# Performance work log

Measured on AMD Instinct MI355X. Metric: run time of the kernel, lower is better.

Reference implementation:

```python
import jax, jax.numpy as jnp
import numpy as np

N, B, S, CIN, E, H = 8192, 4, 2816, 64, 128, 8
HD = E // H


def setup_inputs() -> dict:
    key = jax.random.key(0)
    ks = jax.random.split(key, 8)
    b_ids = jnp.sort(jax.random.randint(ks[0], (N,), 0, B))
    other = jax.random.randint(ks[1], (N, 3), 0, 100)
    voxel_coords = jnp.concatenate([b_ids[:, None], other], axis=1).astype(jnp.int32)
    s = 0.02
    return {
        'pillar_features': jax.random.normal(ks[2], (N, CIN), jnp.float32),
        'voxel_coords': voxel_coords,
        'batch_size': B,
        'max_pillars': S,
        'pre_w': jax.random.normal(ks[3], (CIN, E), jnp.float32) * s,
        'pre_b': jnp.zeros((E,), jnp.float32),
        'in_w': jax.random.normal(ks[4], (E, 3 * E), jnp.float32) * s,
        'in_b': jnp.zeros((3 * E,), jnp.float32),
        'out_w': jax.random.normal(ks[5], (E, E), jnp.float32) * s,
        'out_b': jnp.zeros((E,), jnp.float32),
        'ln1_g': jnp.ones((E,), jnp.float32),
        'ln1_b': jnp.zeros((E,), jnp.float32),
        'w1': jax.random.normal(ks[6], (E, 2 * E), jnp.float32) * s,
        'b1': jnp.zeros((2 * E,), jnp.float32),
        'w2': jax.random.normal(ks[7], (2 * E, E), jnp.float32) * s,
        'b2': jnp.zeros((E,), jnp.float32),
        'ln2_g': jnp.ones((E,), jnp.float32),
        'ln2_b': jnp.zeros((E,), jnp.float32),
    }


def _ln(x, g, b):
    m = jnp.mean(x, axis=-1, keepdims=True)
    v = jnp.var(x, axis=-1, keepdims=True)
    return (x - m) / jnp.sqrt(v + 1e-5) * g + b


def reference(pillar_features, voxel_coords, batch_size, max_pillars,
              pre_w, pre_b, in_w, in_b, out_w, out_b,
              ln1_g, ln1_b, w1, b1, w2, b2, ln2_g, ln2_b):
    n = pillar_features.shape[0]
    b_ids = voxel_coords[:, 0].astype(jnp.int32)
    counts = jax.ops.segment_sum(jnp.ones((n,), jnp.int32), b_ids, num_segments=batch_size)
    starts = jnp.concatenate([jnp.zeros((1,), jnp.int32), jnp.cumsum(counts)[:-1]])
    pos = jnp.arange(n, dtype=jnp.int32) - starts[b_ids]  # index within each batch (coords sorted by batch)

    # pack ragged pillars -> padded [B, S, C]
    padded = jnp.zeros((batch_size, max_pillars, pillar_features.shape[-1]),
                       pillar_features.dtype).at[b_ids, pos].set(pillar_features)
    valid = jnp.arange(max_pillars)[None, :] < counts[:, None]  # [B, S], True = real pillar

    x = padded @ pre_w + pre_b  # [B, S, E]

    # multi-head self-attention with key padding mask
    qkv = x @ in_w + in_b
    q, k, v = jnp.split(qkv, 3, axis=-1)
    def heads(t):
        return t.reshape(batch_size, max_pillars, H, HD).transpose(0, 2, 1, 3)
    q, k, v = heads(q), heads(k), heads(v)
    scores = jnp.einsum('bhqd,bhkd->bhqk', q, k) / jnp.sqrt(jnp.float32(HD))
    scores = scores + jnp.where(valid[:, None, None, :], 0.0, -1e9)
    attn = jax.nn.softmax(scores, axis=-1)
    ctx = jnp.einsum('bhqk,bhkd->bhqd', attn, v)
    ctx = ctx.transpose(0, 2, 1, 3).reshape(batch_size, max_pillars, E)
    attn_out = ctx @ out_w + out_b

    x = _ln(x + attn_out, ln1_g, ln1_b)
    ffn = jax.nn.gelu(x @ w1 + b1, approximate=False) @ w2 + b2
    x = _ln(x + ffn, ln2_g, ln2_b)

    # unpack back to ragged [N_total, E]
    return x[b_ids, pos]
```

## Files before the change

### kernel.cpp

```cpp
#include <hip/hip_runtime.h>
#include <hip/hip_bf16.h>
#include <math.h>

#define CIN 64
#define E   128
#define H3  384
#define FF  256
#define NH  8
#define HD  16
#define NBATCH 4

typedef __attribute__((ext_vector_type(8))) short short8;
typedef __attribute__((ext_vector_type(16))) float f32x16;
typedef __attribute__((ext_vector_type(4))) uint uint4v;

static __device__ __forceinline__ ushort f2bf(float f) {
    uint u = __float_as_uint(f);
    return (ushort)((u + 0x7fffu + ((u >> 16) & 1u)) >> 16);
}
static __device__ __forceinline__ uint f2bf2(float lo, float hi) {
    uint r;
    asm("v_cvt_pk_bf16_f32 %0, %1, %2" : "=v"(r) : "v"(lo), "v"(hi));
    return r;
}
static __device__ __forceinline__ void plswap(uint& a, uint& b) {
    auto r = __builtin_amdgcn_permlane32_swap(a, b, false, false);
    a = r[0]; b = r[1];
}
static __device__ __forceinline__ short8 mk8(uint a, uint b, uint c, uint d) {
    uint4v v; v[0] = a; v[1] = b; v[2] = c; v[3] = d;
    return __builtin_bit_cast(short8, v);
}

__global__ __launch_bounds__(256) void k_wprep(const float* w0, const float* w1, const float* w2,
                                               const float* w3, const float* w4,
                                               ushort* f0, ushort* f1, ushort* f2,
                                               ushort* f3, ushort* f4,
                                               const int* __restrict__ coords, int n,
                                               int* __restrict__ starts) {
    const int m = blockIdx.y;
    const int t = blockIdx.x * 256 + threadIdx.x;
    if (m == 5) {
        if (t >= n) return;
        int cur = coords[t * 4];
        int prev = (t == 0) ? -1 : coords[(t - 1) * 4];
        for (int bb = prev + 1; bb <= cur; ++bb) starts[bb] = t;
        if (t == n - 1)
            for (int bb = cur + 1; bb <= NBATCH; ++bb) starts[bb] = n;
        return;
    }
    const int Ks[5] = {CIN, E, E, E, FF};
    const int Ms[5] = {E, H3, E, FF, E};
    const float* src = m == 0 ? w0 : m == 1 ? w1 : m == 2 ? w2 : m == 3 ? w3 : w4;
    ushort* dst = m == 0 ? f0 : m == 1 ? f1 : m == 2 ? f2 : m == 3 ? f3 : f4;
    const int K = Ks[m], M = Ms[m];
    const int CT = M / 32;
    const int total = (K / 16) * CT * 64;
    if (t >= total) return;
    const int lane = t & 63;
    const int ct = (t >> 6) % CT;
    const int kt = (t >> 6) / CT;
    const int col = ct * 32 + (lane & 31);
    const int k0 = kt * 16 + 8 * (lane >> 5);
    const float* sp = src + (size_t)k0 * M + col;
    uint a = f2bf2(sp[0], sp[(size_t)M]);
    uint b = f2bf2(sp[2 * (size_t)M], sp[3 * (size_t)M]);
    uint c = f2bf2(sp[4 * (size_t)M], sp[5 * (size_t)M]);
    uint d = f2bf2(sp[6 * (size_t)M], sp[7 * (size_t)M]);
    *(short8*)(dst + (size_t)t * 8) = mk8(a, b, c, d);
}

__global__ __launch_bounds__(256) void k_preqkv(const float* __restrict__ feat, const ushort* __restrict__ wf0,
        const float* __restrict__ pre_b, const ushort* __restrict__ wf1, const float* __restrict__ in_b,
        float* __restrict__ x, ushort* __restrict__ qh, ushort* __restrict__ kh, ushort* __restrict__ vt2,
        int n, int npk) {
    __shared__ ushort sxb[32][136];
    __shared__ ushort lv[4][32][34];
    const int rt = blockIdx.x;
    const int NT = n >> 6;
    const int tid = threadIdx.x, w = tid >> 6, lane = tid & 63;
    const int l31 = lane & 31, hi = lane >> 5;
    const int row = rt * 32 + l31;
    const int gt = rt >> 1, halfT = rt & 1;
    const float SC = 0.25f * 1.4426950408889634f;
    {
        const uint ONE2 = 0x3F803F80u;
        for (int it = tid; it < 512; it += 256) {
            const int hh = it >> 6, rloc = (it >> 2) & 15, seg = it & 3;
            *(uint4*)(vt2 + ((size_t)(hh * NT + gt) * 32 + 16 + rloc) * 64 + halfT * 32 + seg * 8) =
                make_uint4(ONE2, ONE2, ONE2, ONE2);
        }
    }
    {
        f32x16 acc;
#pragma unroll
        for (int i = 0; i < 16; ++i) acc[i] = 0.f;
#pragma unroll
        for (int kt = 0; kt < 4; ++kt) {
            const float* ap = feat + (size_t)row * CIN + kt * 16 + 8 * hi;
            const float4 a0 = *(const float4*)ap;
            const float4 a1 = *(const float4*)(ap + 4);
            const short8 af = mk8(f2bf2(a0.x, a0.y), f2bf2(a0.z, a0.w),
                                  f2bf2(a1.x, a1.y), f2bf2(a1.z, a1.w));
            const short8 bf = *(const short8*)(wf0 + ((size_t)(kt * 4 + w) * 64 + lane) * 8);
            acc = __builtin_amdgcn_mfma_f32_32x32x16_bf16(af, bf, acc, 0, 0, 0);
        }
        const int col = w * 32 + l31;
        const float bj = pre_b[col];
#pragma unroll
        for (int r = 0; r < 16; ++r) {
            const int rowl = (r & 3) + 8 * (r >> 2) + 4 * hi;
            const float v = acc[r] + bj;
            x[(size_t)(rt * 32 + rowl) * E + col] = v;
            sxb[rowl][col] = f2bf(v);
        }
    }
    __syncthreads();
#pragma unroll
    for (int c = 0; c < 3; ++c) {
        const int ct = w + 4 * c;
        f32x16 acc;
#pragma unroll
        for (int i = 0; i < 16; ++i) acc[i] = 0.f;
#pragma unroll
        for (int kt = 0; kt < 8; ++kt) {
            const short8 af = *(const short8*)(&sxb[l31][kt * 16 + 8 * hi]);
            const short8 bf = *(const short8*)(wf1 + ((size_t)(kt * 12 + ct) * 64 + lane) * 8);
            acc = __builtin_amdgcn_mfma_f32_32x32x16_bf16(af, bf, acc, 0, 0, 0);
        }
        const int colg = ct * 32 + l31;
        const float bj = in_b[colg];
        if (c == 0) {
            const int hh = colg >> 4, d = colg & 15;
#pragma unroll
            for (int r = 0; r < 16; r += 2) {
                const int rowl = (r & 3) + 8 * (r >> 2) + 4 * hi;
                const int grow = rt * 32 + rowl;
                const uint u = f2bf2((acc[r] + bj) * SC, (acc[r + 1] + bj) * SC);
                qh[((size_t)hh * npk + grow) * 16 + d] = (ushort)u;
                qh[((size_t)hh * npk + grow + 1) * 16 + d] = (ushort)(u >> 16);
            }
        } else if (c == 1) {
            const int cg2 = colg - E;
            const int hh = cg2 >> 4, d = cg2 & 15;
#pragma unroll
            for (int r = 0; r < 16; r += 2) {
                const int rowl = (r & 3) + 8 * (r >> 2) + 4 * hi;
                const int grow = rt * 32 + rowl;
                const uint u = f2bf2(acc[r] + bj, acc[r + 1] + bj);
                kh[((size_t)hh * npk + grow) * 16 + d] = (ushort)u;
                kh[((size_t)hh * npk + grow + 1) * 16 + d] = (ushort)(u >> 16);
            }
        } else {
#pragma unroll
            for (int r = 0; r < 16; ++r) {
                const int rowl = (r & 3) + 8 * (r >> 2) + 4 * hi;
                lv[w][l31][rowl] = f2bf(acc[r] + bj);
            }
            const int d = lane >> 1, half = lane & 1;
            const int dg = (ct - 8) * 32 + d;
            const int hh = dg >> 4, dl = dg & 15;
            const short8 v0 = *(const short8*)(&lv[w][d][16 * half]);
            const short8 v1 = *(const short8*)(&lv[w][d][16 * half + 8]);
            ushort* dst = vt2 + ((size_t)(hh * NT + gt) * 32 + dl) * 64 + halfT * 32 + 16 * half;
            *(short8*)dst = v0;
            *(short8*)(dst + 8) = v1;
        }
    }
}

__global__ __launch_bounds__(256) void k_attn15(const ushort* __restrict__ qh, const ushort* __restrict__ kh,
        const ushort* __restrict__ vt2, const int* __restrict__ starts, ushort* __restrict__ ctxb,
        int n, int npk) {
    __shared__ float po[4][32][17];
    const int NT = n >> 6;
    const int bid = blockIdx.x;
    const int h = bid & 7;
    const int bx = bid >> 3;
    const int tid = threadIdx.x, lane = tid & 63, w = tid >> 6;
    int b = -1, bt = 0, s = 0, e = 0, cum = 0;
    for (int bb = 0; bb < NBATCH; ++bb) {
        int sb = starts[bb], eb = starts[bb + 1];
        int t = (eb - (sb & ~31) + 31) >> 5;
        if (b < 0 && bx < cum + t) { b = bb; bt = bx - cum; s = sb; e = eb; }
        cum += t;
    }
    if (b < 0) return;
    const int q0 = (s & ~31) + bt * 32;
    const int l31 = lane & 31, hi = lane >> 5;
    const short8 qf = *(const short8*)(qh + ((size_t)h * npk + q0 + l31) * 16 + 8 * hi);
    const int ks64 = s & ~63;
    const int ntk = (e - ks64 + 63) >> 6;
    const int tw = (ntk + 3) >> 2;
    const int t0 = w * tw, t1 = min(ntk, t0 + tw);

    f32x16 o, z;
#pragma unroll
    for (int i = 0; i < 16; ++i) { o[i] = 0.f; z[i] = 0.f; }

    const ushort* kbase = kh + ((size_t)h * npk + ks64 + l31) * 16 + 8 * hi;
    const ushort* vbase = vt2 + ((size_t)(h * NT + (ks64 >> 6)) * 32 + l31) * 64 + 8 * hi;

    short8 ck0, ck1, cv0, cv1, cv2, cv3;
    if (t0 < t1) {
        const ushort* kp = kbase + (size_t)t0 * 1024;
        ck0 = *(const short8*)kp;
        ck1 = *(const short8*)(kp + 512);
        const ushort* vp = vbase + (size_t)t0 * 2048;
        cv0 = *(const short8*)(vp);
        cv1 = *(const short8*)(vp + 16);
        cv2 = *(const short8*)(vp + 32);
        cv3 = *(const short8*)(vp + 48);
    }
    for (int tt = t0; tt < t1; ++tt) {
        const int ptn = min(tt + 1, t1 - 1);
        const ushort* kpn = kbase + (size_t)ptn * 1024;
        const short8 nk0 = *(const short8*)kpn;
        const short8 nk1 = *(const short8*)(kpn + 512);
        const ushort* vpn = vbase + (size_t)ptn * 2048;
        const short8 nv0 = *(const short8*)(vpn);
        const short8 nv1 = *(const short8*)(vpn + 16);
        const short8 nv2 = *(const short8*)(vpn + 32);
        const short8 nv3 = *(const short8*)(vpn + 48);
        f32x16 sf0 = __builtin_amdgcn_mfma_f32_32x32x16_bf16(ck0, qf, z, 0, 0, 0);
        f32x16 sf1 = __builtin_amdgcn_mfma_f32_32x32x16_bf16(ck1, qf, z, 0, 0, 0);
        if (tt == 0 || tt == ntk - 1) {
            const int ktg = ks64 + 64 * tt;
#pragma unroll
            for (int r = 0; r < 16; ++r) {
                const int key = ktg + (r & 3) + 8 * (r >> 2) + 4 * hi;
                if (key < s || key >= e) sf0[r] = -1e30f;
                if (key + 32 < s || key + 32 >= e) sf1[r] = -1e30f;
            }
        }
#pragma unroll
        for (int r = 0; r < 16; ++r) sf0[r] = __builtin_amdgcn_exp2f(sf0[r]);
        {
            uint pA0 = f2bf2(sf0[0], sf0[1]),  pA1 = f2bf2(sf0[2], sf0[3]);
            uint pA2 = f2bf2(sf0[4], sf0[5]),  pA3 = f2bf2(sf0[6], sf0[7]);
            uint pA4 = f2bf2(sf0[8], sf0[9]),  pA5 = f2bf2(sf0[10], sf0[11]);
            uint pA6 = f2bf2(sf0[12], sf0[13]), pA7 = f2bf2(sf0[14], sf0[15]);
            plswap(pA0, pA2); plswap(pA1, pA3);
            plswap(pA4, pA6); plswap(pA5, pA7);
            __builtin_amdgcn_s_setprio(1);
            o = __builtin_amdgcn_mfma_f32_32x32x16_bf16(cv0, mk8(pA0, pA1, pA2, pA3), o, 0, 0, 0);
            o = __builtin_amdgcn_mfma_f32_32x32x16_bf16(cv1, mk8(pA4, pA5, pA6, pA7), o, 0, 0, 0);
            __builtin_amdgcn_s_setprio(0);
        }
#pragma unroll
        for (int r = 0; r < 16; ++r) sf1[r] = __builtin_amdgcn_exp2f(sf1[r]);
        {
            uint pB0 = f2bf2(sf1[0], sf1[1]),  pB1 = f2bf2(sf1[2], sf1[3]);
            uint pB2 = f2bf2(sf1[4], sf1[5]),  pB3 = f2bf2(sf1[6], sf1[7]);
            uint pB4 = f2bf2(sf1[8], sf1[9]),  pB5 = f2bf2(sf1[10], sf1[11]);
            uint pB6 = f2bf2(sf1[12], sf1[13]), pB7 = f2bf2(sf1[14], sf1[15]);
            plswap(pB0, pB2); plswap(pB1, pB3);
            plswap(pB4, pB6); plswap(pB5, pB7);
            __builtin_amdgcn_s_setprio(1);
            o = __builtin_amdgcn_mfma_f32_32x32x16_bf16(cv2, mk8(pB0, pB1, pB2, pB3), o, 0, 0, 0);
            o = __builtin_amdgcn_mfma_f32_32x32x16_bf16(cv3, mk8(pB4, pB5, pB6, pB7), o, 0, 0, 0);
            __builtin_amdgcn_s_setprio(0);
        }
        ck0 = nk0; ck1 = nk1;
        cv0 = nv0; cv1 = nv1; cv2 = nv2; cv3 = nv3;
    }
#pragma unroll
    for (int r = 0; r < 8; ++r) {
        const int d = (r & 3) + 8 * (r >> 2) + 4 * hi;
        po[w][l31][d] = o[r];
    }
    if (hi == 0) po[w][l31][16] = o[8];
    __syncthreads();
    const int q = tid & 31, d0 = (tid >> 5) * 2;
    const int rowq = q0 + q;
    if (rowq >= s && rowq < e) {
        float L = 0.f, a0 = 0.f, a1 = 0.f;
#pragma unroll
        for (int ww = 0; ww < 4; ++ww) {
            L += po[ww][q][16];
            a0 += po[ww][q][d0];
            a1 += po[ww][q][d0 + 1];
        }
        const float inv = 1.f / L;
        *(uint*)(ctxb + (size_t)rowq * E + h * HD + d0) = f2bf2(a0 * inv, a1 * inv);
    }
}

__global__ __launch_bounds__(256) void k_post(const ushort* __restrict__ ctxb, const ushort* __restrict__ wf2,
        const float* __restrict__ ob, const float* __restrict__ x,
        const float* __restrict__ g1, const float* __restrict__ be1,
        const ushort* __restrict__ wf3, const float* __restrict__ b1,
        const ushort* __restrict__ wf4, const float* __restrict__ b2,
        const float* __restrict__ g2, const float* __restrict__ be2,
        float* __restrict__ out, int n) {
    __shared__ float ly[32][132];
    __shared__ ushort sxb[32][136];
    __shared__ ushort hbt[32][264];
    const int rt = blockIdx.x;
    const int tid = threadIdx.x, w = tid >> 6, lane = tid & 63;
    const int l31 = lane & 31, hi = lane >> 5;
    const int row = rt * 32 + l31;
    {
        f32x16 acc;
#pragma unroll
        for (int i = 0; i < 16; ++i) acc[i] = 0.f;
#pragma unroll
        for (int kt = 0; kt < 8; ++kt) {
            const short8 af = *(const short8*)(ctxb + (size_t)row * E + kt * 16 + 8 * hi);
            const short8 bf = *(const short8*)(wf2 + ((size_t)(kt * 4 + w) * 64 + lane) * 8);
            acc = __builtin_amdgcn_mfma_f32_32x32x16_bf16(af, bf, acc, 0, 0, 0);
        }
        const int col = w * 32 + l31;
        const float bj = ob[col];
#pragma unroll
        for (int r = 0; r < 16; ++r) {
            const int rowl = (r & 3) + 8 * (r >> 2) + 4 * hi;
            ly[rowl][col] = acc[r] + bj + x[(size_t)(rt * 32 + rowl) * E + col];
        }
    }
    __syncthreads();
    {
        const int r = tid >> 3, j = tid & 7;
        float* lrow = ly[r];
        float v[16];
#pragma unroll
        for (int q = 0; q < 4; ++q) {
            const float4 t = *(const float4*)(lrow + 16 * j + 4 * q);
            v[4 * q] = t.x; v[4 * q + 1] = t.y; v[4 * q + 2] = t.z; v[4 * q + 3] = t.w;
        }
        float s = 0.f, ss = 0.f;
#pragma unroll
        for (int i = 0; i < 16; ++i) { s += v[i]; ss += v[i] * v[i]; }
        for (int m = 1; m < 8; m <<= 1) { s += __shfl_xor(s, m); ss += __shfl_xor(ss, m); }
        const float mean = s * (1.f / 128.f);
        const float var = ss * (1.f / 128.f) - mean * mean;
        const float rstd = rsqrtf(var + 1e-5f);
        float zv[16];
#pragma unroll
        for (int q = 0; q < 4; ++q) {
            const float4 gg = *(const float4*)(g1 + 16 * j + 4 * q);
            const float4 bb = *(const float4*)(be1 + 16 * j + 4 * q);
            zv[4 * q]     = (v[4 * q] - mean) * rstd * gg.x + bb.x;
            zv[4 * q + 1] = (v[4 * q + 1] - mean) * rstd * gg.y + bb.y;
            zv[4 * q + 2] = (v[4 * q + 2] - mean) * rstd * gg.z + bb.z;
            zv[4 * q + 3] = (v[4 * q + 3] - mean) * rstd * gg.w + bb.w;
            *(float4*)(lrow + 16 * j + 4 * q) = make_float4(zv[4 * q], zv[4 * q + 1], zv[4 * q + 2], zv[4 * q + 3]);
        }
        *(uint4*)(&sxb[r][16 * j]) =
            make_uint4(f2bf2(zv[0], zv[1]), f2bf2(zv[2], zv[3]), f2bf2(zv[4], zv[5]), f2bf2(zv[6], zv[7]));
        *(uint4*)(&sxb[r][16 * j + 8]) =
            make_uint4(f2bf2(zv[8], zv[9]), f2bf2(zv[10], zv[11]), f2bf2(zv[12], zv[13]), f2bf2(zv[14], zv[15]));
    }
    __syncthreads();
#pragma unroll
    for (int c = 0; c < 2; ++c) {
        const int ct = w + 4 * c;
        f32x16 acc;
#pragma unroll
        for (int i = 0; i < 16; ++i) acc[i] = 0.f;
#pragma unroll
        for (int kt = 0; kt < 8; ++kt) {
            const short8 af = *(const short8*)(&sxb[l31][kt * 16 + 8 * hi]);
            const short8 bf = *(const short8*)(wf3 + ((size_t)(kt * 8 + ct) * 64 + lane) * 8);
            acc = __builtin_amdgcn_mfma_f32_32x32x16_bf16(af, bf, acc, 0, 0, 0);
        }
        const int col = ct * 32 + l31;
        const float bj = b1[col];
#pragma unroll
        for (int r = 0; r < 16; ++r) {
            const int rowl = (r & 3) + 8 * (r >> 2) + 4 * hi;
            const float vv = acc[r] + bj;
            hbt[rowl][col] = f2bf(0.5f * vv * (1.f + erff(vv * 0.7071067811865475f)));
        }
    }
    __syncthreads();
    float res[16];
    {
        f32x16 acc;
#pragma unroll
        for (int i = 0; i < 16; ++i) acc[i] = 0.f;
#pragma unroll
        for (int kt = 0; kt < 16; ++kt) {
            const short8 af = *(const short8*)(&hbt[l31][kt * 16 + 8 * hi]);
            const short8 bf = *(const short8*)(wf4 + ((size_t)(kt * 4 + w) * 64 + lane) * 8);
            acc = __builtin_amdgcn_mfma_f32_32x32x16_bf16(af, bf, acc, 0, 0, 0);
        }
        const int col = w * 32 + l31;
        const float bj = b2[col];
#pragma unroll
        for (int r = 0; r < 16; ++r) {
            const int rowl = (r & 3) + 8 * (r >> 2) + 4 * hi;
            res[r] = acc[r] + bj + ly[rowl][col];
        }
    }
    __syncthreads();
    {
        const int col = w * 32 + l31;
#pragma unroll
        for (int r = 0; r < 16; ++r) {
            const int rowl = (r & 3) + 8 * (r >> 2) + 4 * hi;
            ly[rowl][col] = res[r];
        }
    }
    __syncthreads();
    {
        const int r = tid >> 3, j = tid & 7;
        const float* lrow = ly[r];
        float v[16];
#pragma unroll
        for (int q = 0; q < 4; ++q) {
            const float4 t = *(const float4*)(lrow + 16 * j + 4 * q);
            v[4 * q] = t.x; v[4 * q + 1] = t.y; v[4 * q + 2] = t.z; v[4 * q + 3] = t.w;
        }
        float s = 0.f, ss = 0.f;
#pragma unroll
        for (int i = 0; i < 16; ++i) { s += v[i]; ss += v[i] * v[i]; }
        for (int m = 1; m < 8; m <<= 1) { s += __shfl_xor(s, m); ss += __shfl_xor(ss, m); }
        const float mean = s * (1.f / 128.f);
        const float var = ss * (1.f / 128.f) - mean * mean;
        const float rstd = rsqrtf(var + 1e-5f);
        const int grow = rt * 32 + r;
#pragma unroll
        for (int q = 0; q < 4; ++q) {
            const float4 gg = *(const float4*)(g2 + 16 * j + 4 * q);
            const float4 bb = *(const float4*)(be2 + 16 * j + 4 * q);
            float4 o;
            o.x = (v[4 * q] - mean) * rstd * gg.x + bb.x;
            o.y = (v[4 * q + 1] - mean) * rstd * gg.y + bb.y;
            o.z = (v[4 * q + 2] - mean) * rstd * gg.z + bb.z;
            o.w = (v[4 * q + 3] - mean) * rstd * gg.w + bb.w;
            *(float4*)(out + (size_t)grow * E + 16 * j + 4 * q) = o;
        }
    }
}

extern "C" void kernel_launch(void* const* d_in, const int* in_sizes, int n_in,
                              void* d_out, int out_size, void* d_ws, size_t ws_size,
                              hipStream_t stream) {
    const float* feat   = (const float*)d_in[0];
    const int*   coords = (const int*)d_in[1];
    const float* pre_w  = (const float*)d_in[4];
    const float* pre_b  = (const float*)d_in[5];
    const float* in_w   = (const float*)d_in[6];
    const float* in_b   = (const float*)d_in[7];
    const float* out_w  = (const float*)d_in[8];
    const float* out_b  = (const float*)d_in[9];
    const float* ln1_g  = (const float*)d_in[10];
    const float* ln1_b  = (const float*)d_in[11];
    const float* w1     = (const float*)d_in[12];
    const float* b1     = (const float*)d_in[13];
    const float* w2     = (const float*)d_in[14];
    const float* b2     = (const float*)d_in[15];
    const float* ln2_g  = (const float*)d_in[16];
    const float* ln2_b  = (const float*)d_in[17];
    float* out = (float*)d_out;

    const int n = in_sizes[0] / CIN;
    const int RT = n / 32;
    const int npk = n + 64;
    const int NT = n / 64;

    char* wsb = (char*)d_ws;
    int* starts = (int*)wsb;
    float* x    = (float*)(wsb + 256);
    ushort* qh  = (ushort*)(x + (size_t)n * E);
    ushort* kh  = qh + (size_t)NH * npk * 16;
    ushort* vt2 = kh + (size_t)NH * npk * 16;
    ushort* ctxb = vt2 + (size_t)NH * NT * 32 * 64;
    ushort* wf0 = ctxb + (size_t)n * E;
    ushort* wf1 = wf0 + 4 * 4 * 64 * 8;
    ushort* wf2 = wf1 + 8 * 12 * 64 * 8;
    ushort* wf3 = wf2 + 8 * 4 * 64 * 8;
    ushort* wf4 = wf3 + 8 * 8 * 64 * 8;

    k_wprep<<<dim3(32, 6), dim3(256), 0, stream>>>(pre_w, in_w, out_w, w1, w2,
                                                   wf0, wf1, wf2, wf3, wf4, coords, n, starts);
    k_preqkv<<<dim3(RT), dim3(256), 0, stream>>>(feat, wf0, pre_b, wf1, in_b, x, qh, kh, vt2, n, npk);
    k_attn15<<<dim3((n / 32 + NBATCH) * NH), dim3(256), 0, stream>>>(qh, kh, vt2, starts, ctxb, n, npk);
    k_post<<<dim3(RT), dim3(256), 0, stream>>>(ctxb, wf2, out_b, x, ln1_g, ln1_b,
                                               wf3, b1, wf4, b2, ln2_g, ln2_b, out, n);
}
```

Measured before the change: 78.48 us.

## Restructure V tile layout into per-slice blocks and drop register prefetch

Changes the transposed V buffer layout so each 16-key slice of a 64-key tile sits in its own contiguous 32x16 block. Each wavefront's V fragment loads then read contiguous 512-byte spans instead of strided 128-byte rows. The attention loop also drops its software double-buffered register prefetch of K/V in favour of direct loads each iteration. That lowers register pressure but exposes load latency unless the compiler or occupancy hides it.

```diff
diff --git a/kernel.cpp b/kernel.cpp
--- a/kernel.cpp
+++ b/kernel.cpp
@@ -86,8 +86,10 @@
     {
         const uint ONE2 = 0x3F803F80u;
         for (int it = tid; it < 512; it += 256) {
-            const int hh = it >> 6, rloc = (it >> 2) & 15, seg = it & 3;
-            *(uint4*)(vt2 + ((size_t)(hh * NT + gt) * 32 + 16 + rloc) * 64 + halfT * 32 + seg * 8) =
+            const int hh = it >> 6, rem = it & 63;
+            const int sl = 2 * halfT + (rem >> 5);
+            const int rloc = (rem >> 1) & 15, seg = rem & 1;
+            *(uint4*)(vt2 + (((size_t)(hh * NT + gt) * 4 + sl) * 32 + 16 + rloc) * 16 + seg * 8) =
                 make_uint4(ONE2, ONE2, ONE2, ONE2);
         }
     }
@@ -160,16 +162,17 @@
             const int d = lane >> 1, half = lane & 1;
             const int dg = (ct - 8) * 32 + d;
             const int hh = dg >> 4, dl = dg & 15;
+            const int sl = 2 * halfT + half;
             const short8 v0 = *(const short8*)(&lv[w][d][16 * half]);
             const short8 v1 = *(const short8*)(&lv[w][d][16 * half + 8]);
-            ushort* dst = vt2 + ((size_t)(hh * NT + gt) * 32 + dl) * 64 + halfT * 32 + 16 * half;
+            ushort* dst = vt2 + (((size_t)(hh * NT + gt) * 4 + sl) * 32 + dl) * 16;
             *(short8*)dst = v0;
             *(short8*)(dst + 8) = v1;
         }
     }
 }
 
-__global__ __launch_bounds__(256) void k_attn15(const ushort* __restrict__ qh, const ushort* __restrict__ kh,
+__global__ __launch_bounds__(256) void k_attn17(const ushort* __restrict__ qh, const ushort* __restrict__ kh,
         const ushort* __restrict__ vt2, const int* __restrict__ starts, ushort* __restrict__ ctxb,
         int n, int npk) {
     __shared__ float po[4][32][17];
@@ -199,29 +202,17 @@
     for (int i = 0; i < 16; ++i) { o[i] = 0.f; z[i] = 0.f; }
 
     const ushort* kbase = kh + ((size_t)h * npk + ks64 + l31) * 16 + 8 * hi;
-    const ushort* vbase = vt2 + ((size_t)(h * NT + (ks64 >> 6)) * 32 + l31) * 64 + 8 * hi;
-
-    short8 ck0, ck1, cv0, cv1, cv2, cv3;
-    if (t0 < t1) {
-        const ushort* kp = kbase + (size_t)t0 * 1024;
-        ck0 = *(const short8*)kp;
-        ck1 = *(const short8*)(kp + 512);
-        const ushort* vp = vbase + (size_t)t0 * 2048;
-        cv0 = *(const short8*)(vp);
-        cv1 = *(const short8*)(vp + 16);
-        cv2 = *(const short8*)(vp + 32);
-        cv3 = *(const short8*)(vp + 48);
-    }
+    const ushort* vbase = vt2 + (size_t)(h * NT + (ks64 >> 6)) * 2048 + l31 * 16 + 8 * hi;
+
     for (int tt = t0; tt < t1; ++tt) {
-        const int ptn = min(tt + 1, t1 - 1);
-        const ushort* kpn = kbase + (size_t)ptn * 1024;
-        const short8 nk0 = *(const short8*)kpn;
-        const short8 nk1 = *(const short8*)(kpn + 512);
-        const ushort* vpn = vbase + (size_t)ptn * 2048;
-        const short8 nv0 = *(const short8*)(vpn);
-        const short8 nv1 = *(const short8*)(vpn + 16);
-        const short8 nv2 = *(const short8*)(vpn + 32);
-        const short8 nv3 = *(const short8*)(vpn + 48);
+        const ushort* kp = kbase + (size_t)tt * 1024;
+        const short8 ck0 = *(const short8*)kp;
+        const short8 ck1 = *(const short8*)(kp + 512);
+        const ushort* vt = vbase + (size_t)tt * 2048;
+        const short8 vf0 = *(const short8*)(vt);
+        const short8 vf1 = *(const short8*)(vt + 512);
+        const short8 vf2 = *(const short8*)(vt + 1024);
+        const short8 vf3 = *(const short8*)(vt + 1536);
         f32x16 sf0 = __builtin_amdgcn_mfma_f32_32x32x16_bf16(ck0, qf, z, 0, 0, 0);
         f32x16 sf1 = __builtin_amdgcn_mfma_f32_32x32x16_bf16(ck1, qf, z, 0, 0, 0);
         if (tt == 0 || tt == ntk - 1) {
@@ -243,8 +234,8 @@
             plswap(pA0, pA2); plswap(pA1, pA3);
             plswap(pA4, pA6); plswap(pA5, pA7);
             __builtin_amdgcn_s_setprio(1);
-            o = __builtin_amdgcn_mfma_f32_32x32x16_bf16(cv0, mk8(pA0, pA1, pA2, pA3), o, 0, 0, 0);
-            o = __builtin_amdgcn_mfma_f32_32x32x16_bf16(cv1, mk8(pA4, pA5, pA6, pA7), o, 0, 0, 0);
+            o = __builtin_amdgcn_mfma_f32_32x32x16_bf16(vf0, mk8(pA0, pA1, pA2, pA3), o, 0, 0, 0);
+            o = __builtin_amdgcn_mfma_f32_32x32x16_bf16(vf1, mk8(pA4, pA5, pA6, pA7), o, 0, 0, 0);
             __builtin_amdgcn_s_setprio(0);
         }
 #pragma unroll
@@ -257,12 +248,10 @@
             plswap(pB0, pB2); plswap(pB1, pB3);
             plswap(pB4, pB6); plswap(pB5, pB7);
             __builtin_amdgcn_s_setprio(1);
-            o = __builtin_amdgcn_mfma_f32_32x32x16_bf16(cv2, mk8(pB0, pB1, pB2, pB3), o, 0, 0, 0);
-            o = __builtin_amdgcn_mfma_f32_32x32x16_bf16(cv3, mk8(pB4, pB5, pB6, pB7), o, 0, 0, 0);
+            o = __builtin_amdgcn_mfma_f32_32x32x16_bf16(vf2, mk8(pB0, pB1, pB2, pB3), o, 0, 0, 0);
+            o = __builtin_amdgcn_mfma_f32_32x32x16_bf16(vf3, mk8(pB4, pB5, pB6, pB7), o, 0, 0, 0);
             __builtin_amdgcn_s_setprio(0);
         }
-        ck0 = nk0; ck1 = nk1;
-        cv0 = nv0; cv1 = nv1; cv2 = nv2; cv3 = nv3;
     }
 #pragma unroll
     for (int r = 0; r < 8; ++r) {
@@ -466,7 +455,7 @@
     ushort* qh  = (ushort*)(x + (size_t)n * E);
     ushort* kh  = qh + (size_t)NH * npk * 16;
     ushort* vt2 = kh + (size_t)NH * npk * 16;
-    ushort* ctxb = vt2 + (size_t)NH * NT * 32 * 64;
+    ushort* ctxb = vt2 + (size_t)NH * NT * 2048;
     ushort* wf0 = ctxb + (size_t)n * E;
     ushort* wf1 = wf0 + 4 * 4 * 64 * 8;
     ushort* wf2 = wf1 + 8 * 12 * 64 * 8;
@@ -476,7 +465,7 @@
     k_wprep<<<dim3(32, 6), dim3(256), 0, stream>>>(pre_w, in_w, out_w, w1, w2,
                                                    wf0, wf1, wf2, wf3, wf4, coords, n, starts);
     k_preqkv<<<dim3(RT), dim3(256), 0, stream>>>(feat, wf0, pre_b, wf1, in_b, x, qh, kh, vt2, n, npk);
-    k_attn15<<<dim3((n / 32 + NBATCH) * NH), dim3(256), 0, stream>>>(qh, kh, vt2, starts, ctxb, n, npk);
+    k_attn17<<<dim3((n / 32 + NBATCH) * NH), dim3(256), 0, stream>>>(qh, kh, vt2, starts, ctxb, n, npk);
     k_post<<<dim3(RT), dim3(256), 0, stream>>>(ctxb, wf2, out_b, x, ln1_g, ln1_b,
                                                wf3, b1, wf4, b2, ln2_g, ln2_b, out, n);
 }
```

Measured after the change: 64.51 us (median of 2 runs). -17.8%, faster.
